# Performance work log

Hardware: AMD Instinct MI355X
Metric: run time of the kernel (lower is better)

## Reference

```python
import jax, jax.numpy as jnp
import numpy as np

WS = 16
NB = 800
THRESH = 0.05


def setup_inputs() -> dict:
    key = jax.random.key(0)
    k1, k2, k3, k4 = jax.random.split(key, 4)
    tensor_msi = jax.random.uniform(k1, (1, 64, 512, 512), dtype=jnp.float32)
    tensor_he = jax.random.uniform(k2, (1, 3, 512, 512), dtype=jnp.float32)
    i_idx = jax.random.randint(k3, (NB,), 0, 512 - WS, dtype=jnp.int32)
    j_idx = jax.random.randint(k4, (NB,), 0, 512 - WS, dtype=jnp.int32)
    return {
        "tensor_msi": tensor_msi,
        "tensor_he": tensor_he,
        "i_idx": i_idx,
        "j_idx": j_idx,
        "window_size": WS,
        "batch": NB,
    }


def reference(tensor_msi, tensor_he, i_idx, j_idx, window_size, batch):
    u = tensor_msi.shape[1]
    msi = tensor_msi[:, : u // 2]  # only first half of MSI channels is used
    ws = window_size
    p = ws * ws

    def get_patch(x, i, j):
        # x: [1, C, M, N] -> [C, ws*ws]
        c = x.shape[1]
        patch = jax.lax.dynamic_slice(x, (0, 0, i, j), (1, c, ws, ws))
        return patch.reshape(c, p)

    def pdist2(x, mask):
        # pairwise squared L2 distance over positions: D[a,b] = sum_k (x[k,a]-x[k,b])^2
        sq = jnp.sum(x * x, axis=0)  # [p]
        gram = jnp.einsum("kp,kq->pq", x, x)  # [p, p]
        d = sq[:, None] + sq[None, :] - 2.0 * gram
        # zero out rows/cols where the HE patch intensity sum < THRESH
        return d * mask[:, None] * mask[None, :]

    def per_patch(i, j):
        pm = get_patch(msi, i, j)  # [u//2, p]
        ph = get_patch(tensor_he, i, j)  # [3, p]
        # NOTE: original code computes index_zero from MSI then overwrites it
        # with the HE-based one; only the HE mask is applied to both.
        mask = (jnp.sum(ph, axis=0) >= THRESH).astype(pm.dtype)  # [p]
        dm = pdist2(pm, mask)
        dh = jax.lax.stop_gradient(pdist2(ph, mask))  # .detach()
        return jnp.mean(jnp.abs(dm - dh))  # L1Loss mean

    losses = jax.vmap(per_patch)(i_idx, j_idx)  # [batch]
    return jnp.sum(losses) / (batch // 5)
```

## Files before the change

kernel.cpp:

```cpp
#include <hip/hip_runtime.h>
#include <hip/hip_bf16.h>


#define WS   16
#define PSZ  256
#define IMG  512
#define IMG2 (IMG * IMG)
#define XSTR 40

typedef __attribute__((ext_vector_type(8))) short short8;
typedef __attribute__((ext_vector_type(4))) float float4v;

static __device__ __forceinline__ unsigned short f2bf(float v) {
    union { __hip_bfloat16 b; unsigned short u; } cv;
    cv.b = __float2bfloat16(v);
    return cv.u;
}
static __device__ __forceinline__ float bf2f(unsigned short u) {
    union { unsigned int u; float f; } cv;
    cv.u = ((unsigned int)u) << 16;
    return cv.f;
}

__global__ __launch_bounds__(256, 2)
void corr_loss_kernel(const float* __restrict__ msi,
                      const float* __restrict__ he,
                      const int* __restrict__ i_idx,
                      const int* __restrict__ j_idx,
                      float* __restrict__ out,
                      float scale)
{
    __shared__ __align__(16) unsigned short xs[PSZ * XSTR];
    __shared__ __align__(16) unsigned short heA[PSZ * 8];
    __shared__ __align__(16) unsigned short heB[PSZ * 8];
    __shared__ __align__(16) unsigned int   zq[4];
    __shared__ __align__(16) float s_lds[PSZ];
    __shared__ __align__(16) float m_lds[PSZ];
    __shared__ float red[4];

    const int b = blockIdx.x;
    const int t = threadIdx.x;
    const int i0 = i_idx[b], j0 = j_idx[b];

    {
        const int r = t >> 4, c = t & 15;
        const float* mp = msi + (size_t)(i0 + r) * IMG + (j0 + c);
        float sm = 0.f;
#pragma unroll
        for (int g = 0; g < 4; ++g) {
            float v[8];
#pragma unroll
            for (int k = 0; k < 8; ++k) v[k] = mp[(size_t)(g * 8 + k) * IMG2];
            unsigned int pk[4];
#pragma unroll
            for (int k = 0; k < 4; ++k) {
                unsigned short lo = f2bf(v[2 * k]), hi = f2bf(v[2 * k + 1]);
                float fl = bf2f(lo), fh = bf2f(hi);
                sm = fmaf(fl, fl, sm);
                sm = fmaf(fh, fh, sm);
                pk[k] = (unsigned int)lo | ((unsigned int)hi << 16);
            }
            *(uint4*)&xs[t * XSTR + g * 8] = make_uint4(pk[0], pk[1], pk[2], pk[3]);
        }
        const float* hp = he + (size_t)(i0 + r) * IMG + (j0 + c);
        float hsum = 0.f, sh = 0.f;
        unsigned short hb[3];
#pragma unroll
        for (int ch = 0; ch < 3; ++ch) {
            float hv = hp[(size_t)ch * IMG2];
            hsum += hv;
            hb[ch] = f2bf(hv);
            float hr = bf2f(hb[ch]);
            sh = fmaf(hr, hr, sh);
        }
        *(uint4*)&heB[t * 8] =
            make_uint4((unsigned)hb[0] | ((unsigned)hb[1] << 16), (unsigned)hb[2], 0u, 0u);
        unsigned short n0 = hb[0] ^ 0x8000u, n1 = hb[1] ^ 0x8000u, n2 = hb[2] ^ 0x8000u;
        *(uint4*)&heA[t * 8] =
            make_uint4((unsigned)n0 | ((unsigned)n1 << 16), (unsigned)n2, 0u, 0u);
        s_lds[t] = sm - sh;
        m_lds[t] = (hsum >= 0.05f) ? 1.f : 0.f;
        if (t < 4) zq[t] = 0u;
    }
    __syncthreads();

    const int lane = t & 63, w = t >> 6;
    const int m = lane & 15, quad = lane >> 4;
    const short8* zfrag = (const short8*)zq;

    short8  Am[4], Ah[4];
    float4v sr4[4], mr4[4];
#pragma unroll
    for (int ii = 0; ii < 4; ++ii) {
        const int ri = (w * 4 + ii) * 16;
        Am[ii]  = *(const short8*)&xs[(ri + m) * XSTR + quad * 8];
        Ah[ii]  = (quad == 0) ? *(const short8*)&heA[(ri + m) * 8] : *zfrag;
        sr4[ii] = *(const float4v*)&s_lds[ri + quad * 4];
        mr4[ii] = *(const float4v*)&m_lds[ri + quad * 4];
    }

    float accv[4] = {0.f, 0.f, 0.f, 0.f};
#pragma unroll 2
    for (int j = 0; j < 16; ++j) {
        const int cj = j * 16;
        short8 Bm = *(const short8*)&xs[(cj + m) * XSTR + quad * 8];
        short8 Bh = (quad == 0) ? *(const short8*)&heB[(cj + m) * 8] : *zfrag;
        float  sc = s_lds[cj + m];
        float  mc = m_lds[cj + m];
#pragma unroll
        for (int ii = 0; ii < 4; ++ii) {
            float4v g = {0.f, 0.f, 0.f, 0.f};
            g = __builtin_amdgcn_mfma_f32_16x16x32_bf16(Ah[ii], Bh, g, 0, 0, 0);
            g = __builtin_amdgcn_mfma_f32_16x16x32_bf16(Am[ii], Bm, g, 0, 0, 0);
#pragma unroll
            for (int reg = 0; reg < 4; ++reg) {
                float tt = sr4[ii][reg] + sc;
                float rr = fmaf(-2.f, g[reg], tt);
                accv[ii] = fmaf(mr4[ii][reg] * mc, fabsf(rr), accv[ii]);
            }
        }
    }
    float acc = (accv[0] + accv[1]) + (accv[2] + accv[3]);

#pragma unroll
    for (int off = 32; off > 0; off >>= 1)
        acc += __shfl_down(acc, off, 64);
    if (lane == 0) red[w] = acc;
    __syncthreads();
    if (t == 0)
        atomicAdd(out, (red[0] + red[1] + red[2] + red[3]) * scale);
}

extern "C" void kernel_launch(void* const* d_in, const int* in_sizes, int n_in,
                              void* d_out, int out_size, void* d_ws, size_t ws_size,
                              hipStream_t stream) {
    const float* msi   = (const float*)d_in[0];
    const float* he    = (const float*)d_in[1];
    const int*   i_idx = (const int*)d_in[2];
    const int*   j_idx = (const int*)d_in[3];
    const int    NB    = in_sizes[2];
    float*       out   = (float*)d_out;

    hipMemsetAsync(out, 0, sizeof(float) * out_size, stream);

    const float scale = 1.0f / ((float)(PSZ * PSZ) * (float)(NB / 5));
    corr_loss_kernel<<<NB, 256, 0, stream>>>(msi, he, i_idx, j_idx, out, scale);
}
```

Before: 113.2 us.

## Exploit distance-matrix symmetry: compute only upper-triangle tiles, double off-diagonal

Measured after the change: 115.3 us. About the same (+1.8%).

```diff
diff --git a/kernel.cpp b/kernel.cpp
--- a/kernel.cpp
+++ b/kernel.cpp
@@ -22,7 +22,7 @@
     return cv.f;
 }
 
-__global__ __launch_bounds__(256, 2)
+__global__ __launch_bounds__(256, 4)
 void corr_loss_kernel(const float* __restrict__ msi,
                       const float* __restrict__ he,
                       const int* __restrict__ i_idx,
@@ -86,41 +86,48 @@
 
     const int lane = t & 63, w = t >> 6;
     const int m = lane & 15, quad = lane >> 4;
-    const short8* zfrag = (const short8*)zq;
+    const short8 zfrag = *(const short8*)zq;
 
-    short8  Am[4], Ah[4];
-    float4v sr4[4], mr4[4];
+    float accD = 0.f, accO = 0.f;
+
+    int l = 0;
+    for (int ti = 0; ti < 16; ++ti) {
+        const int cnt = 16 - ti;
+        const int r = (w - l) & 3;
+        if (r < cnt) {
+            const int ri = ti << 4;
+            short8  Am  = *(const short8*)&xs[(ri + m) * XSTR + (quad << 3)];
+            short8  Ah  = (quad == 0) ? *(const short8*)&heA[(ri + m) << 3] : zfrag;
+            float4v sr4 = *(const float4v*)&s_lds[ri + (quad << 2)];
+            float4v mr4 = *(const float4v*)&m_lds[ri + (quad << 2)];
+
+            auto tile = [&](int tj) -> float {
+                const int cj = tj << 4;
+                short8 Bm = *(const short8*)&xs[(cj + m) * XSTR + (quad << 3)];
+                short8 Bh = (quad == 0) ? *(const short8*)&heB[(cj + m) << 3] : zfrag;
+                float  sc = s_lds[cj + m];
+                float  mc = m_lds[cj + m];
+                float4v g = {0.f, 0.f, 0.f, 0.f};
+                g = __builtin_amdgcn_mfma_f32_16x16x32_bf16(Ah, Bh, g, 0, 0, 0);
+                g = __builtin_amdgcn_mfma_f32_16x16x32_bf16(Am, Bm, g, 0, 0, 0);
+                float lacc = 0.f;
 #pragma unroll
-    for (int ii = 0; ii < 4; ++ii) {
-        const int ri = (w * 4 + ii) * 16;
-        Am[ii]  = *(const short8*)&xs[(ri + m) * XSTR + quad * 8];
-        Ah[ii]  = (quad == 0) ? *(const short8*)&heA[(ri + m) * 8] : *zfrag;
-        sr4[ii] = *(const float4v*)&s_lds[ri + quad * 4];
-        mr4[ii] = *(const float4v*)&m_lds[ri + quad * 4];
+                for (int reg = 0; reg < 4; ++reg) {
+                    float tt = sr4[reg] + sc;
+                    float rr = fmaf(-2.f, g[reg], tt);
+                    lacc = fmaf(mr4[reg] * mc, fabsf(rr), lacc);
+                }
+                return lacc;
+            };
+
+            int tj = ti + r;
+            if (r == 0) { accD += tile(ti); tj += 4; }
+            for (; tj < 16; tj += 4) accO += tile(tj);
+        }
+        l += cnt;
     }
 
-    float accv[4] = {0.f, 0.f, 0.f, 0.f};
-#pragma unroll 2
-    for (int j = 0; j < 16; ++j) {
-        const int cj = j * 16;
-        short8 Bm = *(const short8*)&xs[(cj + m) * XSTR + quad * 8];
-        short8 Bh = (quad == 0) ? *(const short8*)&heB[(cj + m) * 8] : *zfrag;
-        float  sc = s_lds[cj + m];
-        float  mc = m_lds[cj + m];
-#pragma unroll
-        for (int ii = 0; ii < 4; ++ii) {
-            float4v g = {0.f, 0.f, 0.f, 0.f};
-            g = __builtin_amdgcn_mfma_f32_16x16x32_bf16(Ah[ii], Bh, g, 0, 0, 0);
-            g = __builtin_amdgcn_mfma_f32_16x16x32_bf16(Am[ii], Bm, g, 0, 0, 0);
-#pragma unroll
-            for (int reg = 0; reg < 4; ++reg) {
-                float tt = sr4[ii][reg] + sc;
-                float rr = fmaf(-2.f, g[reg], tt);
-                accv[ii] = fmaf(mr4[ii][reg] * mc, fabsf(rr), accv[ii]);
-            }
-        }
-    }
-    float acc = (accv[0] + accv[1]) + (accv[2] + accv[3]);
+    float acc = fmaf(2.f, accO, accD);
 
 #pragma unroll
     for (int off = 32; off > 0; off >>= 1)
```

## Fold norms, mask and -2 factor into augmented MFMA operands

Applied to the files above, without the earlier changes.

Measured after the change: 111.8 us. Within noise of the previous version (-1.2%).

```diff
diff --git a/kernel.cpp b/kernel.cpp
--- a/kernel.cpp
+++ b/kernel.cpp
@@ -2,7 +2,6 @@
 #include <hip/hip_bf16.h>
 
 
-#define WS   16
 #define PSZ  256
 #define IMG  512
 #define IMG2 (IMG * IMG)
@@ -22,7 +21,7 @@
     return cv.f;
 }
 
-__global__ __launch_bounds__(256, 2)
+__global__ __launch_bounds__(256, 4)
 void corr_loss_kernel(const float* __restrict__ msi,
                       const float* __restrict__ he,
                       const int* __restrict__ i_idx,
@@ -31,11 +30,8 @@
                       float scale)
 {
     __shared__ __align__(16) unsigned short xs[PSZ * XSTR];
-    __shared__ __align__(16) unsigned short heA[PSZ * 8];
-    __shared__ __align__(16) unsigned short heB[PSZ * 8];
-    __shared__ __align__(16) unsigned int   zq[4];
-    __shared__ __align__(16) float s_lds[PSZ];
-    __shared__ __align__(16) float m_lds[PSZ];
+    __shared__ __align__(16) unsigned short eA[PSZ * 8];
+    __shared__ __align__(16) unsigned short eB[PSZ * 8];
     __shared__ float red[4];
 
     const int b = blockIdx.x;
@@ -44,17 +40,23 @@
 
     {
         const int r = t >> 4, c = t & 15;
+        const float* hp = he + (size_t)(i0 + r) * IMG + (j0 + c);
+        const float h0 = hp[0], h1 = hp[IMG2], h2 = hp[2 * IMG2];
+        const float mf = (h0 + h1 + h2 >= 0.05f) ? 1.f : 0.f;
+        const unsigned short hb0 = f2bf(h0 * mf), hb1 = f2bf(h1 * mf), hb2 = f2bf(h2 * mf);
+        const float hr0 = bf2f(hb0), hr1 = bf2f(hb1), hr2 = bf2f(hb2);
+        const float sh = hr0 * hr0 + hr1 * hr1 + hr2 * hr2;
+
         const float* mp = msi + (size_t)(i0 + r) * IMG + (j0 + c);
         float sm = 0.f;
 #pragma unroll
         for (int g = 0; g < 4; ++g) {
-            float v[8];
-#pragma unroll
-            for (int k = 0; k < 8; ++k) v[k] = mp[(size_t)(g * 8 + k) * IMG2];
             unsigned int pk[4];
 #pragma unroll
             for (int k = 0; k < 4; ++k) {
-                unsigned short lo = f2bf(v[2 * k]), hi = f2bf(v[2 * k + 1]);
+                float v0 = mp[(size_t)(g * 8 + 2 * k)     * IMG2] * mf;
+                float v1 = mp[(size_t)(g * 8 + 2 * k + 1) * IMG2] * mf;
+                unsigned short lo = f2bf(v0), hi = f2bf(v1);
                 float fl = bf2f(lo), fh = bf2f(hi);
                 sm = fmaf(fl, fl, sm);
                 sm = fmaf(fh, fh, sm);
@@ -62,70 +64,70 @@
             }
             *(uint4*)&xs[t * XSTR + g * 8] = make_uint4(pk[0], pk[1], pk[2], pk[3]);
         }
-        const float* hp = he + (size_t)(i0 + r) * IMG + (j0 + c);
-        float hsum = 0.f, sh = 0.f;
-        unsigned short hb[3];
-#pragma unroll
-        for (int ch = 0; ch < 3; ++ch) {
-            float hv = hp[(size_t)ch * IMG2];
-            hsum += hv;
-            hb[ch] = f2bf(hv);
-            float hr = bf2f(hb[ch]);
-            sh = fmaf(hr, hr, sh);
-        }
-        *(uint4*)&heB[t * 8] =
-            make_uint4((unsigned)hb[0] | ((unsigned)hb[1] << 16), (unsigned)hb[2], 0u, 0u);
-        unsigned short n0 = hb[0] ^ 0x8000u, n1 = hb[1] ^ 0x8000u, n2 = hb[2] ^ 0x8000u;
-        *(uint4*)&heA[t * 8] =
-            make_uint4((unsigned)n0 | ((unsigned)n1 << 16), (unsigned)n2, 0u, 0u);
-        s_lds[t] = sm - sh;
-        m_lds[t] = (hsum >= 0.05f) ? 1.f : 0.f;
-        if (t < 4) zq[t] = 0u;
+        const float s = sm - sh;
+        const unsigned short shi = f2bf(s);
+        const unsigned short slo = f2bf(s - bf2f(shi));
+        const unsigned short mb  = (mf != 0.f) ? (unsigned short)0x3F80 : (unsigned short)0;
+        const unsigned short d0  = f2bf(2.f * hr0);
+        const unsigned short d1  = f2bf(2.f * hr1);
+        const unsigned short d2  = f2bf(2.f * hr2);
+        *(uint4*)&eA[t * 8] = make_uint4(
+            (unsigned)d0 | ((unsigned)d1 << 16),
+            (unsigned)d2 | ((unsigned)shi << 16),
+            (unsigned)slo | ((unsigned)mb << 16),
+            (unsigned)mb);
+        *(uint4*)&eB[t * 8] = make_uint4(
+            (unsigned)hb0 | ((unsigned)hb1 << 16),
+            (unsigned)hb2 | ((unsigned)mb << 16),
+            (unsigned)mb | ((unsigned)shi << 16),
+            (unsigned)slo);
     }
     __syncthreads();
 
     const int lane = t & 63, w = t >> 6;
-    const int m = lane & 15, quad = lane >> 4;
-    const short8* zfrag = (const short8*)zq;
+    const int mrow = lane & 15, quad = lane >> 4;
+    const short8 zfrag = {0, 0, 0, 0, 0, 0, 0, 0};
 
-    short8  Am[4], Ah[4];
-    float4v sr4[4], mr4[4];
+    short8 Am[4], Ah[4];
 #pragma unroll
     for (int ii = 0; ii < 4; ++ii) {
-        const int ri = (w * 4 + ii) * 16;
-        Am[ii]  = *(const short8*)&xs[(ri + m) * XSTR + quad * 8];
-        Ah[ii]  = (quad == 0) ? *(const short8*)&heA[(ri + m) * 8] : *zfrag;
-        sr4[ii] = *(const float4v*)&s_lds[ri + quad * 4];
-        mr4[ii] = *(const float4v*)&m_lds[ri + quad * 4];
+        const int ri = ((w << 2) + ii) * 16 + mrow;
+        uint4 u = *(const uint4*)&xs[ri * XSTR + (quad << 3)];
+        u.x = (u.x ^ 0x80008000u) + 0x00800080u;
+        u.y = (u.y ^ 0x80008000u) + 0x00800080u;
+        u.z = (u.z ^ 0x80008000u) + 0x00800080u;
+        u.w = (u.w ^ 0x80008000u) + 0x00800080u;
+        Am[ii] = *(const short8*)&u;
+        Ah[ii] = (quad == 0) ? *(const short8*)&eA[ri << 3] : zfrag;
     }
 
-    float accv[4] = {0.f, 0.f, 0.f, 0.f};
-#pragma unroll 2
+    float acc[4] = {0.f, 0.f, 0.f, 0.f};
+#pragma unroll 4
     for (int j = 0; j < 16; ++j) {
-        const int cj = j * 16;
-        short8 Bm = *(const short8*)&xs[(cj + m) * XSTR + quad * 8];
-        short8 Bh = (quad == 0) ? *(const short8*)&heB[(cj + m) * 8] : *zfrag;
-        float  sc = s_lds[cj + m];
-        float  mc = m_lds[cj + m];
+        const int cj = (j << 4) + mrow;
+        short8 Bm = *(const short8*)&xs[cj * XSTR + (quad << 3)];
+        short8 Bh = (quad == 0) ? *(const short8*)&eB[cj << 3] : zfrag;
+        float4v g[4];
 #pragma unroll
         for (int ii = 0; ii < 4; ++ii) {
-            float4v g = {0.f, 0.f, 0.f, 0.f};
-            g = __builtin_amdgcn_mfma_f32_16x16x32_bf16(Ah[ii], Bh, g, 0, 0, 0);
-            g = __builtin_amdgcn_mfma_f32_16x16x32_bf16(Am[ii], Bm, g, 0, 0, 0);
+            g[ii] = (float4v){0.f, 0.f, 0.f, 0.f};
+            g[ii] = __builtin_amdgcn_mfma_f32_16x16x32_bf16(Ah[ii], Bh, g[ii], 0, 0, 0);
+            g[ii] = __builtin_amdgcn_mfma_f32_16x16x32_bf16(Am[ii], Bm, g[ii], 0, 0, 0);
+        }
 #pragma unroll
-            for (int reg = 0; reg < 4; ++reg) {
-                float tt = sr4[ii][reg] + sc;
-                float rr = fmaf(-2.f, g[reg], tt);
-                accv[ii] = fmaf(mr4[ii][reg] * mc, fabsf(rr), accv[ii]);
-            }
+        for (int ii = 0; ii < 4; ++ii) {
+            acc[ii] += fabsf(g[ii][0]);
+            acc[ii] += fabsf(g[ii][1]);
+            acc[ii] += fabsf(g[ii][2]);
+            acc[ii] += fabsf(g[ii][3]);
         }
     }
-    float acc = (accv[0] + accv[1]) + (accv[2] + accv[3]);
+    float a = (acc[0] + acc[1]) + (acc[2] + acc[3]);
 
 #pragma unroll
     for (int off = 32; off > 0; off >>= 1)
-        acc += __shfl_down(acc, off, 64);
-    if (lane == 0) red[w] = acc;
+        a += __shfl_down(a, off, 64);
+    if (lane == 0) red[w] = a;
     __syncthreads();
     if (t == 0)
         atomicAdd(out, (red[0] + red[1] + red[2] + red[3]) * scale);
```
